# Kernel tuning notes

Hardware: AMD Instinct MI355X
Metric: run time of the kernel (lower is better)

## Reference

```python
import jax, jax.numpy as jnp
import numpy as np

B, N_GENES, N_SETS, G = 256, 10000, 1000, 128   # batch, input_dim, output_dim, geneset_size
H1, H2 = 64, 32                                  # hidden_dims
EPS = 1e-5                                       # BatchNorm1d eps


def _batchnorm(h, gamma, beta):
    # BatchNorm1d in training mode: biased batch stats over the batch axis
    mean = jnp.mean(h, axis=0, keepdims=True)
    var = jnp.mean(jnp.square(h - mean), axis=0, keepdims=True)
    return (h - mean) * jax.lax.rsqrt(var + EPS) * gamma + beta


def setup_inputs() -> dict:
    key = jax.random.key(0)
    ks = jax.random.split(key, 7)
    # Adjacency with exactly G distinct ones per column -> gather index list [N_SETS, G]
    rng = np.random.default_rng(0)
    gene_idx = np.argsort(rng.random((N_SETS, N_GENES)), axis=1)[:, :G]
    gene_idx = jnp.asarray(np.sort(gene_idx, axis=1), dtype=jnp.int32)

    x = jax.random.normal(ks[0], (B, N_GENES), jnp.float32)
    s1, s2, s3 = 1.0 / np.sqrt(G), 1.0 / np.sqrt(H1), 1.0 / np.sqrt(H2)
    W1 = jax.random.uniform(ks[1], (N_SETS, G, H1), jnp.float32, -s1, s1)
    b1 = jax.random.uniform(ks[2], (N_SETS, H1), jnp.float32, -s1, s1)
    W2 = jax.random.uniform(ks[3], (N_SETS, H1, H2), jnp.float32, -s2, s2)
    b2 = jax.random.uniform(ks[4], (N_SETS, H2), jnp.float32, -s2, s2)
    W3 = jax.random.uniform(ks[5], (N_SETS, H2), jnp.float32, -s3, s3)
    b3 = jax.random.uniform(ks[6], (N_SETS,), jnp.float32, -s3, s3)
    g1 = jnp.ones((N_SETS, H1), jnp.float32)
    be1 = jnp.zeros((N_SETS, H1), jnp.float32)
    g2 = jnp.ones((N_SETS, H2), jnp.float32)
    be2 = jnp.zeros((N_SETS, H2), jnp.float32)
    return {"x": x, "gene_idx": gene_idx, "W1": W1, "b1": b1, "g1": g1, "be1": be1,
            "W2": W2, "b2": b2, "g2": g2, "be2": be2, "W3": W3, "b3": b3}


def reference(x, gene_idx, W1, b1, g1, be1, W2, b2, g2, be2, W3, b3):
    # Per-geneset gather: x[:, adj[:,i]==1] for all i at once -> [B, S, G]
    xg = x[:, gene_idx]
    # Linear -> ReLU -> BatchNorm (per geneset, grouped GEMM)
    h = jax.nn.relu(jnp.einsum('bsg,sgh->bsh', xg, W1) + b1)
    h = _batchnorm(h, g1, be1)
    h = jax.nn.relu(jnp.einsum('bsh,shk->bsk', h, W2) + b2)
    h = _batchnorm(h, g2, be2)
    # Final Linear(H2 -> 1) -> ReLU, concatenated over genesets -> [B, S]
    out = jax.nn.relu(jnp.einsum('bsh,sh->bs', h, W3) + b3)
    return out
```

## Files before the change

### kernel.cpp

```cpp
#include <hip/hip_runtime.h>
#include <stdint.h>

#define BB 256
#define NG 10000
#define NS 1000
#define GG 128
#define H1 64
#define H2 32
#define EPSV 1e-5f


typedef unsigned short ushortT;
typedef __attribute__((ext_vector_type(4))) short short4v;
typedef __attribute__((ext_vector_type(8))) short short8v;
typedef __attribute__((ext_vector_type(4))) float float4v;

__device__ __forceinline__ float bf2f(ushortT u) {
    union { uint32_t i; float f; } v; v.i = ((uint32_t)u) << 16; return v.f;
}
__device__ __forceinline__ ushortT f2bf(float f) {
    union { float f; uint32_t i; } v; v.f = f;
    uint32_t x = v.i;
    return (ushortT)((x + 0x7fffu + ((x >> 16) & 1u)) >> 16);
}
__device__ __forceinline__ uint32_t pack2(ushortT lo, ushortT hi) {
    return (uint32_t)lo | ((uint32_t)hi << 16);
}
__device__ __forceinline__ bool probe_f32(const void* g1) {
    return ((*(const uint32_t*)g1) & 0xFFFFu) == 0u;
}
__device__ __forceinline__ float loadf(const void* p, int i, bool isf) {
    return isf ? ((const float*)p)[i] : bf2f(((const ushortT*)p)[i]);
}
__device__ __forceinline__ ushortT loadbf(const void* p, size_t i, bool isf) {
    return isf ? f2bf(((const float*)p)[i]) : ((const ushortT*)p)[i];
}

__global__ __launch_bounds__(256) void k_transpose(const void* __restrict__ x,
                                                   ushortT* __restrict__ xT,
                                                   const void* __restrict__ g1p) {
    __shared__ ushortT tile[64][66];
    const bool isf = probe_f32(g1p);
    const int tx = threadIdx.x & 63;
    const int tz = threadIdx.x >> 6;
    const int j0 = blockIdx.x * 64;
    const int b0 = blockIdx.y * 64;
    const int j = j0 + tx;
#pragma unroll
    for (int k = 0; k < 16; ++k) {
        int bl = tz * 16 + k;
        ushortT v = 0;
        if (j < NG) v = loadbf(x, (size_t)(b0 + bl) * NG + j, isf);
        tile[bl][tx] = v;
    }
    __syncthreads();
#pragma unroll
    for (int k = 0; k < 16; ++k) {
        int jl = tz * 16 + k;
        int jw = j0 + jl;
        if (jw < NG) xT[jw * BB + b0 + tx] = tile[tx][jl];
    }
}

__global__ __launch_bounds__(256, 3) void k_main(
    const ushortT* __restrict__ xT, const int* __restrict__ gidx,
    const void* __restrict__ W1, const void* __restrict__ W2,
    const void* __restrict__ b1, const void* __restrict__ g1, const void* __restrict__ be1,
    const void* __restrict__ b2, const void* __restrict__ g2, const void* __restrict__ be2,
    const void* __restrict__ W3, const void* __restrict__ b3,
    void* __restrict__ out) {
    __shared__ ushortT xg[BB * 72];
    __shared__ ushortT w1s[H1 * 132];

    char* xgc = (char*)xg;
    float* colA  = (float*)w1s;
    float* colB  = colA + 64;
    float* colA2 = colB + 64;
    float* colB2 = colA2 + 32;
    ushortT* w2s = w1s + 1408;

    const bool isf = probe_f32(g1);
    const int s = blockIdx.x;
    const int t = threadIdx.x;
    const int w = t >> 6;
    const int lane = t & 63;
    const int l16 = lane & 15;
    const int quad = lane >> 4;
    const size_t base1 = (size_t)s * (GG * H1);
    const size_t base2 = (size_t)s * (H1 * H2);

    float b1v[4], w3v[2], b2v[2];
#pragma unroll
    for (int nt = 0; nt < 4; ++nt) b1v[nt] = loadf(b1, s * H1 + nt * 16 + l16, isf);
#pragma unroll
    for (int nt = 0; nt < 2; ++nt) {
        b2v[nt] = loadf(b2, s * H2 + nt * 16 + l16, isf);
        w3v[nt] = loadf(W3, s * H2 + nt * 16 + l16, isf);
    }
    const float b3v = loadf(b3, s, isf);
    float g1v = 0.f, be1v = 0.f, g2v = 0.f, be2v = 0.f;
    if (t < 64) { g1v = loadf(g1, s * H1 + t, isf); be1v = loadf(be1, s * H1 + t, isf); }
    if (t < 32) { g2v = loadf(g2, s * H2 + t, isf); be2v = loadf(be2, s * H2 + t, isf); }

    ushortT w2r[8];
    {
        const int k2 = t & 31, h0 = (t >> 5) * 8;
#pragma unroll
        for (int j = 0; j < 8; ++j) w2r[j] = loadbf(W2, base2 + (size_t)(h0 + j) * H2 + k2, isf);
    }

    if (t < GG) *(int*)(xgc + (t >> 2) * 144 + 128 + (t & 3) * 4) = gidx[s * GG + t];

    if (isf) {
        const float4* src = (const float4*)((const float*)W1 + base1);
#pragma unroll
        for (int rep = 0; rep < 8; ++rep) {
            const int e4 = rep * 256 + t;
            const int g = e4 >> 4;
            const int h0 = (e4 & 15) * 4;
            float4 v = src[e4];
            w1s[(h0 + 0) * 132 + g] = f2bf(v.x);
            w1s[(h0 + 1) * 132 + g] = f2bf(v.y);
            w1s[(h0 + 2) * 132 + g] = f2bf(v.z);
            w1s[(h0 + 3) * 132 + g] = f2bf(v.w);
        }
    } else {
        const uint2* src = (const uint2*)((const ushortT*)W1 + base1);
#pragma unroll
        for (int rep = 0; rep < 8; ++rep) {
            const int e4 = rep * 256 + t;
            const int g = e4 >> 4;
            const int h0 = (e4 & 15) * 4;
            uint2 v = src[e4];
            w1s[(h0 + 0) * 132 + g] = (ushortT)v.x;
            w1s[(h0 + 1) * 132 + g] = (ushortT)(v.x >> 16);
            w1s[(h0 + 2) * 132 + g] = (ushortT)v.y;
            w1s[(h0 + 3) * 132 + g] = (ushortT)(v.y >> 16);
        }
    }
    __syncthreads();

    float4v acc1[4][4];
#pragma unroll
    for (int mt = 0; mt < 4; ++mt)
#pragma unroll
        for (int nt = 0; nt < 4; ++nt) acc1[mt][nt] = (float4v){0.f, 0.f, 0.f, 0.f};

#pragma unroll
    for (int c = 0; c < 2; ++c) {
#pragma unroll
        for (int gq = 0; gq < 8; ++gq) {
            const int r0 = c * 16 + gq * 2;
            int4 ia = *(const int4*)(xgc + r0 * 144 + 128);
            int4 ib = *(const int4*)(xgc + (r0 + 1) * 144 + 128);
            ushortT v0 = xT[ia.x * BB + t], v1 = xT[ia.y * BB + t];
            ushortT v2 = xT[ia.z * BB + t], v3 = xT[ia.w * BB + t];
            ushortT v4 = xT[ib.x * BB + t], v5 = xT[ib.y * BB + t];
            ushortT v6 = xT[ib.z * BB + t], v7 = xT[ib.w * BB + t];
            uint4 pk;
            pk.x = pack2(v0, v1);
            pk.y = pack2(v2, v3);
            pk.z = pack2(v4, v5);
            pk.w = pack2(v6, v7);
            *(uint4*)(&xg[t * 72 + gq * 8]) = pk;
        }
#pragma unroll
        for (int kt = 0; kt < 2; ++kt) {
            const int kl = kt * 32 + quad * 8;
            short8v bfrag[4];
#pragma unroll
            for (int nt = 0; nt < 4; ++nt) {
                const int h = nt * 16 + l16;
                const int woff = h * 132 + c * 64 + kl;
                short4v blo = *(const short4v*)(&w1s[woff]);
                short4v bhi = *(const short4v*)(&w1s[woff + 4]);
                bfrag[nt] = __builtin_shufflevector(blo, bhi, 0, 1, 2, 3, 4, 5, 6, 7);
            }
#pragma unroll
            for (int mt = 0; mt < 4; ++mt) {
                const int b = w * 64 + mt * 16 + l16;
                short8v af = *(const short8v*)(&xg[b * 72 + kl]);
#pragma unroll
                for (int nt = 0; nt < 4; ++nt)
                    acc1[mt][nt] = __builtin_amdgcn_mfma_f32_16x16x32_bf16(af, bfrag[nt], acc1[mt][nt], 0, 0, 0);
            }
        }
    }

#pragma unroll
    for (int nt = 0; nt < 4; ++nt) {
        float s1 = 0.f, s2 = 0.f;
        const float bb = b1v[nt];
#pragma unroll
        for (int mt = 0; mt < 4; ++mt)
#pragma unroll
            for (int r = 0; r < 4; ++r) {
                float v = acc1[mt][nt][r] + bb;
                v = v > 0.f ? v : 0.f;
                s1 += v;
                s2 += v * v;
            }
        s1 += __shfl_xor(s1, 16); s1 += __shfl_xor(s1, 32);
        s2 += __shfl_xor(s2, 16); s2 += __shfl_xor(s2, 32);
        if (lane < 16) {
            const int k = w * 64 + nt * 16 + lane;
            *(float*)(xgc + (32 + (k >> 2)) * 144 + 128 + (k & 3) * 4) = s1;
            *(float*)(xgc + (96 + (k >> 2)) * 144 + 128 + (k & 3) * 4) = s2;
        }
    }
    __syncthreads();

    if (t < 64) {
        float ts = 0.f, tq = 0.f;
#pragma unroll
        for (int ww = 0; ww < 4; ++ww) {
            const int k = ww * 64 + t;
            ts += *(const float*)(xgc + (32 + (k >> 2)) * 144 + 128 + (k & 3) * 4);
            tq += *(const float*)(xgc + (96 + (k >> 2)) * 144 + 128 + (k & 3) * 4);
        }
        float mean = ts * (1.0f / 256.0f);
        float var = tq * (1.0f / 256.0f) - mean * mean;
        var = var > 0.f ? var : 0.f;
        float rs = rsqrtf(var + EPSV);
        float a = g1v * rs;
        colA[t] = a;
        colB[t] = be1v - mean * a;
    }
    {
        const int k2 = t & 31, h0 = (t >> 5) * 8;
        uint4 pk;
        pk.x = pack2(w2r[0], w2r[1]);
        pk.y = pack2(w2r[2], w2r[3]);
        pk.z = pack2(w2r[4], w2r[5]);
        pk.w = pack2(w2r[6], w2r[7]);
        *(uint4*)(&w2s[k2 * 72 + h0]) = pk;
    }
    __syncthreads();

#pragma unroll
    for (int nt = 0; nt < 4; ++nt) {
        const int h = nt * 16 + l16;
        const float bb = b1v[nt], a = colA[h], cc = colB[h];
#pragma unroll
        for (int mt = 0; mt < 4; ++mt)
#pragma unroll
            for (int r = 0; r < 4; ++r) {
                const int b = w * 64 + mt * 16 + quad * 4 + r;
                float v = acc1[mt][nt][r] + bb;
                v = v > 0.f ? v : 0.f;
                xg[b * 72 + h] = f2bf(v * a + cc);
            }
    }

    float4v acc2[4][2];
#pragma unroll
    for (int mt = 0; mt < 4; ++mt)
#pragma unroll
        for (int nt = 0; nt < 2; ++nt) acc2[mt][nt] = (float4v){0.f, 0.f, 0.f, 0.f};

#pragma unroll
    for (int kt = 0; kt < 2; ++kt) {
        const int kl = kt * 32 + quad * 8;
        short8v bfrag2[2];
#pragma unroll
        for (int nt = 0; nt < 2; ++nt) {
            const int k2 = nt * 16 + l16;
            bfrag2[nt] = *(const short8v*)(&w2s[k2 * 72 + kl]);
        }
#pragma unroll
        for (int mt = 0; mt < 4; ++mt) {
            const int b = w * 64 + mt * 16 + l16;
            short8v af = *(const short8v*)(&xg[b * 72 + kl]);
#pragma unroll
            for (int nt = 0; nt < 2; ++nt)
                acc2[mt][nt] = __builtin_amdgcn_mfma_f32_16x16x32_bf16(af, bfrag2[nt], acc2[mt][nt], 0, 0, 0);
        }
    }

#pragma unroll
    for (int nt = 0; nt < 2; ++nt) {
        float s1 = 0.f, s2 = 0.f;
        const float bb = b2v[nt];
#pragma unroll
        for (int mt = 0; mt < 4; ++mt)
#pragma unroll
            for (int r = 0; r < 4; ++r) {
                float v = acc2[mt][nt][r] + bb;
                v = v > 0.f ? v : 0.f;
                s1 += v;
                s2 += v * v;
            }
        s1 += __shfl_xor(s1, 16); s1 += __shfl_xor(s1, 32);
        s2 += __shfl_xor(s2, 16); s2 += __shfl_xor(s2, 32);
        if (lane < 16) {
            const int k = w * 64 + nt * 16 + lane;
            *(float*)(xgc + (32 + (k >> 2)) * 144 + 128 + (k & 3) * 4) = s1;
            *(float*)(xgc + (96 + (k >> 2)) * 144 + 128 + (k & 3) * 4) = s2;
        }
    }
    __syncthreads();

    if (t < 32) {
        float ts = 0.f, tq = 0.f;
#pragma unroll
        for (int ww = 0; ww < 4; ++ww) {
            const int k = ww * 64 + t;
            ts += *(const float*)(xgc + (32 + (k >> 2)) * 144 + 128 + (k & 3) * 4);
            tq += *(const float*)(xgc + (96 + (k >> 2)) * 144 + 128 + (k & 3) * 4);
        }
        float mean = ts * (1.0f / 256.0f);
        float var = tq * (1.0f / 256.0f) - mean * mean;
        var = var > 0.f ? var : 0.f;
        float rs = rsqrtf(var + EPSV);
        float a = g2v * rs;
        colA2[t] = a;
        colB2[t] = be2v - mean * a;
    }
    __syncthreads();

    float a2[2], c2[2];
#pragma unroll
    for (int nt = 0; nt < 2; ++nt) {
        const int k2 = nt * 16 + l16;
        a2[nt] = colA2[k2];
        c2[nt] = colB2[k2];
    }
#pragma unroll
    for (int mt = 0; mt < 4; ++mt)
#pragma unroll
        for (int r = 0; r < 4; ++r) {
            float tot = 0.f;
#pragma unroll
            for (int nt = 0; nt < 2; ++nt) {
                float v = acc2[mt][nt][r] + b2v[nt];
                v = v > 0.f ? v : 0.f;
                tot += (v * a2[nt] + c2[nt]) * w3v[nt];
            }
            tot += __shfl_xor(tot, 1);
            tot += __shfl_xor(tot, 2);
            tot += __shfl_xor(tot, 4);
            tot += __shfl_xor(tot, 8);
            if (l16 == 0) {
                const int b = w * 64 + mt * 16 + quad * 4 + r;
                float o = tot + b3v;
                o = o > 0.f ? o : 0.f;
                if (isf) ((float*)out)[b * NS + s] = o;
                else     ((ushortT*)out)[b * NS + s] = f2bf(o);
            }
        }
}

extern "C" void kernel_launch(void* const* d_in, const int* in_sizes, int n_in,
                              void* d_out, int out_size, void* d_ws, size_t ws_size,
                              hipStream_t stream) {
    const int* gi = (const int*)d_in[1];
    ushortT* xT = (ushortT*)d_ws;

    dim3 gT((NG + 63) / 64, BB / 64);
    k_transpose<<<gT, 256, 0, stream>>>(d_in[0], xT, d_in[4]);
    k_main<<<NS, 256, 0, stream>>>(xT, gi, d_in[2], d_in[6],
                                   d_in[3], d_in[4], d_in[5],
                                   d_in[7], d_in[8], d_in[9], d_in[10], d_in[11],
                                   d_out);
}
```

Baseline: 147.7 us.

## Shrink LDS footprint by staging W1 in K-quarters to raise occupancy

Reduces shared memory per block by staging W1 into LDS one 32-wide K slice at a time instead of all 128, and narrowing the xg row pitch from 72 to 68. Reduction scratch moves into the padding holes of the xg rows and into the reused W1 buffer. Launch bounds go from 3 to 4 blocks per CU to exploit the smaller footprint. In exchange there are extra __syncthreads and global W1 reloads inside the K loop, plus split 8-byte LDS reads where 16-byte reads were used before.

Result: faster. 141.9 us (-3.9%).

```diff
diff --git a/kernel.cpp b/kernel.cpp
--- a/kernel.cpp
+++ b/kernel.cpp
@@ -62,22 +62,19 @@
     }
 }
 
-__global__ __launch_bounds__(256, 3) void k_main(
+__global__ __launch_bounds__(256, 4) void k_main(
     const ushortT* __restrict__ xT, const int* __restrict__ gidx,
     const void* __restrict__ W1, const void* __restrict__ W2,
     const void* __restrict__ b1, const void* __restrict__ g1, const void* __restrict__ be1,
     const void* __restrict__ b2, const void* __restrict__ g2, const void* __restrict__ be2,
     const void* __restrict__ W3, const void* __restrict__ b3,
     void* __restrict__ out) {
-    __shared__ ushortT xg[BB * 72];
-    __shared__ ushortT w1s[H1 * 132];
+    __shared__ ushortT xg[BB * 68];
+    __shared__ ushortT w1s[64 * 36];
 
     char* xgc = (char*)xg;
-    float* colA  = (float*)w1s;
-    float* colB  = colA + 64;
-    float* colA2 = colB + 64;
-    float* colB2 = colA2 + 32;
-    ushortT* w2s = w1s + 1408;
+    float* redf = (float*)w1s;
+    ushortT* w2s = w1s;
 
     const bool isf = probe_f32(g1);
     const int s = blockIdx.x;
@@ -89,6 +86,9 @@
     const size_t base1 = (size_t)s * (GG * H1);
     const size_t base2 = (size_t)s * (H1 * H2);
 
+#define HOLEI(i)   (*(int*)(xgc + ((i) >> 1) * 136 + 128 + ((i) & 1) * 4))
+#define HOLEF(r0, k) (*(float*)(xgc + ((r0) + ((k) >> 1)) * 136 + 128 + ((k) & 1) * 4))
+
     float b1v[4], w3v[2], b2v[2];
 #pragma unroll
     for (int nt = 0; nt < 4; ++nt) b1v[nt] = loadf(b1, s * H1 + nt * 16 + l16, isf);
@@ -109,35 +109,31 @@
         for (int j = 0; j < 8; ++j) w2r[j] = loadbf(W2, base2 + (size_t)(h0 + j) * H2 + k2, isf);
     }
 
-    if (t < GG) *(int*)(xgc + (t >> 2) * 144 + 128 + (t & 3) * 4) = gidx[s * GG + t];
-
-    if (isf) {
-        const float4* src = (const float4*)((const float*)W1 + base1);
-#pragma unroll
-        for (int rep = 0; rep < 8; ++rep) {
-            const int e4 = rep * 256 + t;
-            const int g = e4 >> 4;
-            const int h0 = (e4 & 15) * 4;
-            float4 v = src[e4];
-            w1s[(h0 + 0) * 132 + g] = f2bf(v.x);
-            w1s[(h0 + 1) * 132 + g] = f2bf(v.y);
-            w1s[(h0 + 2) * 132 + g] = f2bf(v.z);
-            w1s[(h0 + 3) * 132 + g] = f2bf(v.w);
-        }
-    } else {
-        const uint2* src = (const uint2*)((const ushortT*)W1 + base1);
-#pragma unroll
-        for (int rep = 0; rep < 8; ++rep) {
-            const int e4 = rep * 256 + t;
-            const int g = e4 >> 4;
-            const int h0 = (e4 & 15) * 4;
-            uint2 v = src[e4];
-            w1s[(h0 + 0) * 132 + g] = (ushortT)v.x;
-            w1s[(h0 + 1) * 132 + g] = (ushortT)(v.x >> 16);
-            w1s[(h0 + 2) * 132 + g] = (ushortT)v.y;
-            w1s[(h0 + 3) * 132 + g] = (ushortT)(v.y >> 16);
-        }
-    }
+    if (t < GG) HOLEI(t) = gidx[s * GG + t];
+
+    auto stageW1 = [&](int q) {
+#pragma unroll
+        for (int rep = 0; rep < 2; ++rep) {
+            const int el = rep * 256 + t;
+            const int e4 = q * 512 + el;
+            const int g = el >> 4;
+            const int h0 = (el & 15) * 4;
+            ushortT u0, u1, u2, u3;
+            if (isf) {
+                float4 v = *(const float4*)((const float*)W1 + base1 + (size_t)e4 * 4);
+                u0 = f2bf(v.x); u1 = f2bf(v.y); u2 = f2bf(v.z); u3 = f2bf(v.w);
+            } else {
+                uint2 v = *(const uint2*)((const ushortT*)W1 + base1 + (size_t)e4 * 4);
+                u0 = (ushortT)v.x; u1 = (ushortT)(v.x >> 16);
+                u2 = (ushortT)v.y; u3 = (ushortT)(v.y >> 16);
+            }
+            w1s[(h0 + 0) * 36 + g] = u0;
+            w1s[(h0 + 1) * 36 + g] = u1;
+            w1s[(h0 + 2) * 36 + g] = u2;
+            w1s[(h0 + 3) * 36 + g] = u3;
+        }
+    };
+    stageW1(0);
     __syncthreads();
 
     float4v acc1[4][4];
@@ -150,28 +146,33 @@
     for (int c = 0; c < 2; ++c) {
 #pragma unroll
         for (int gq = 0; gq < 8; ++gq) {
-            const int r0 = c * 16 + gq * 2;
-            int4 ia = *(const int4*)(xgc + r0 * 144 + 128);
-            int4 ib = *(const int4*)(xgc + (r0 + 1) * 144 + 128);
-            ushortT v0 = xT[ia.x * BB + t], v1 = xT[ia.y * BB + t];
-            ushortT v2 = xT[ia.z * BB + t], v3 = xT[ia.w * BB + t];
-            ushortT v4 = xT[ib.x * BB + t], v5 = xT[ib.y * BB + t];
-            ushortT v6 = xT[ib.z * BB + t], v7 = xT[ib.w * BB + t];
-            uint4 pk;
-            pk.x = pack2(v0, v1);
-            pk.y = pack2(v2, v3);
-            pk.z = pack2(v4, v5);
-            pk.w = pack2(v6, v7);
-            *(uint4*)(&xg[t * 72 + gq * 8]) = pk;
+            const int i0 = c * 64 + gq * 8;
+            int2 p0 = *(const int2*)(xgc + (i0 >> 1) * 136 + 128);
+            int2 p1 = *(const int2*)(xgc + ((i0 >> 1) + 1) * 136 + 128);
+            int2 p2 = *(const int2*)(xgc + ((i0 >> 1) + 2) * 136 + 128);
+            int2 p3 = *(const int2*)(xgc + ((i0 >> 1) + 3) * 136 + 128);
+            ushortT v0 = xT[p0.x * BB + t], v1 = xT[p0.y * BB + t];
+            ushortT v2 = xT[p1.x * BB + t], v3 = xT[p1.y * BB + t];
+            ushortT v4 = xT[p2.x * BB + t], v5 = xT[p2.y * BB + t];
+            ushortT v6 = xT[p3.x * BB + t], v7 = xT[p3.y * BB + t];
+            uint2 pa = {pack2(v0, v1), pack2(v2, v3)};
+            uint2 pb = {pack2(v4, v5), pack2(v6, v7)};
+            *(uint2*)(&xg[t * 68 + gq * 8]) = pa;
+            *(uint2*)(&xg[t * 68 + gq * 8 + 4]) = pb;
         }
 #pragma unroll
         for (int kt = 0; kt < 2; ++kt) {
-            const int kl = kt * 32 + quad * 8;
+            const int q = 2 * c + kt;
+            if (q > 0) {
+                __syncthreads();
+                stageW1(q);
+                __syncthreads();
+            }
             short8v bfrag[4];
 #pragma unroll
             for (int nt = 0; nt < 4; ++nt) {
                 const int h = nt * 16 + l16;
-                const int woff = h * 132 + c * 64 + kl;
+                const int woff = h * 36 + quad * 8;
                 short4v blo = *(const short4v*)(&w1s[woff]);
                 short4v bhi = *(const short4v*)(&w1s[woff + 4]);
                 bfrag[nt] = __builtin_shufflevector(blo, bhi, 0, 1, 2, 3, 4, 5, 6, 7);
@@ -179,7 +180,10 @@
 #pragma unroll
             for (int mt = 0; mt < 4; ++mt) {
                 const int b = w * 64 + mt * 16 + l16;
-                short8v af = *(const short8v*)(&xg[b * 72 + kl]);
+                const ushortT* p = &xg[b * 68 + kt * 32 + quad * 8];
+                short4v alo = *(const short4v*)(p);
+                short4v ahi = *(const short4v*)(p + 4);
+                short8v af = __builtin_shufflevector(alo, ahi, 0, 1, 2, 3, 4, 5, 6, 7);
 #pragma unroll
                 for (int nt = 0; nt < 4; ++nt)
                     acc1[mt][nt] = __builtin_amdgcn_mfma_f32_16x16x32_bf16(af, bfrag[nt], acc1[mt][nt], 0, 0, 0);
@@ -187,6 +191,7 @@
         }
     }
 
+    float s1v[4], s2v[4];
 #pragma unroll
     for (int nt = 0; nt < 4; ++nt) {
         float s1 = 0.f, s2 = 0.f;
@@ -202,30 +207,32 @@
             }
         s1 += __shfl_xor(s1, 16); s1 += __shfl_xor(s1, 32);
         s2 += __shfl_xor(s2, 16); s2 += __shfl_xor(s2, 32);
-        if (lane < 16) {
+        s1v[nt] = s1; s2v[nt] = s2;
+    }
+    __syncthreads();
+    if (lane < 16) {
+#pragma unroll
+        for (int nt = 0; nt < 4; ++nt) {
             const int k = w * 64 + nt * 16 + lane;
-            *(float*)(xgc + (32 + (k >> 2)) * 144 + 128 + (k & 3) * 4) = s1;
-            *(float*)(xgc + (96 + (k >> 2)) * 144 + 128 + (k & 3) * 4) = s2;
+            redf[k] = s1v[nt];
+            redf[256 + k] = s2v[nt];
         }
     }
     __syncthreads();
 
     if (t < 64) {
-        float ts = 0.f, tq = 0.f;
-#pragma unroll
-        for (int ww = 0; ww < 4; ++ww) {
-            const int k = ww * 64 + t;
-            ts += *(const float*)(xgc + (32 + (k >> 2)) * 144 + 128 + (k & 3) * 4);
-            tq += *(const float*)(xgc + (96 + (k >> 2)) * 144 + 128 + (k & 3) * 4);
-        }
+        float ts = redf[t] + redf[64 + t] + redf[128 + t] + redf[192 + t];
+        float tq = redf[256 + t] + redf[320 + t] + redf[384 + t] + redf[448 + t];
         float mean = ts * (1.0f / 256.0f);
         float var = tq * (1.0f / 256.0f) - mean * mean;
         var = var > 0.f ? var : 0.f;
         float rs = rsqrtf(var + EPSV);
         float a = g1v * rs;
-        colA[t] = a;
-        colB[t] = be1v - mean * a;
-    }
+        HOLEF(64, t) = a;
+        HOLEF(96, t) = be1v - mean * a;
+    }
+    __syncthreads();
+
     {
         const int k2 = t & 31, h0 = (t >> 5) * 8;
         uint4 pk;
@@ -235,12 +242,11 @@
         pk.w = pack2(w2r[6], w2r[7]);
         *(uint4*)(&w2s[k2 * 72 + h0]) = pk;
     }
-    __syncthreads();
-
 #pragma unroll
     for (int nt = 0; nt < 4; ++nt) {
         const int h = nt * 16 + l16;
-        const float bb = b1v[nt], a = colA[h], cc = colB[h];
+        const float bb = b1v[nt];
+        const float a = HOLEF(64, h), cc = HOLEF(96, h);
 #pragma unroll
         for (int mt = 0; mt < 4; ++mt)
 #pragma unroll
@@ -248,9 +254,10 @@
                 const int b = w * 64 + mt * 16 + quad * 4 + r;
                 float v = acc1[mt][nt][r] + bb;
                 v = v > 0.f ? v : 0.f;
-                xg[b * 72 + h] = f2bf(v * a + cc);
-            }
-    }
+                xg[b * 68 + h] = f2bf(v * a + cc);
+            }
+    }
+    __syncthreads();
 
     float4v acc2[4][2];
 #pragma unroll
@@ -265,12 +272,18 @@
 #pragma unroll
         for (int nt = 0; nt < 2; ++nt) {
             const int k2 = nt * 16 + l16;
-            bfrag2[nt] = *(const short8v*)(&w2s[k2 * 72 + kl]);
+            const int woff = k2 * 72 + kl;
+            short4v blo = *(const short4v*)(&w2s[woff]);
+            short4v bhi = *(const short4v*)(&w2s[woff + 4]);
+            bfrag2[nt] = __builtin_shufflevector(blo, bhi, 0, 1, 2, 3, 4, 5, 6, 7);
         }
 #pragma unroll
         for (int mt = 0; mt < 4; ++mt) {
             const int b = w * 64 + mt * 16 + l16;
-            short8v af = *(const short8v*)(&xg[b * 72 + kl]);
+            const ushortT* p = &xg[b * 68 + kl];
+            short4v alo = *(const short4v*)(p);
+            short4v ahi = *(const short4v*)(p + 4);
+            short8v af = __builtin_shufflevector(alo, ahi, 0, 1, 2, 3, 4, 5, 6, 7);
 #pragma unroll
             for (int nt = 0; nt < 2; ++nt)
                 acc2[mt][nt] = __builtin_amdgcn_mfma_f32_16x16x32_bf16(af, bfrag2[nt], acc2[mt][nt], 0, 0, 0);
@@ -293,28 +306,23 @@
         s1 += __shfl_xor(s1, 16); s1 += __shfl_xor(s1, 32);
         s2 += __shfl_xor(s2, 16); s2 += __shfl_xor(s2, 32);
         if (lane < 16) {
-            const int k = w * 64 + nt * 16 + lane;
-            *(float*)(xgc + (32 + (k >> 2)) * 144 + 128 + (k & 3) * 4) = s1;
-            *(float*)(xgc + (96 + (k >> 2)) * 144 + 128 + (k & 3) * 4) = s2;
+            const int k = w * 32 + nt * 16 + lane;
+            HOLEF(0, k) = s1;
+            HOLEF(64, k) = s2;
         }
     }
     __syncthreads();
 
     if (t < 32) {
-        float ts = 0.f, tq = 0.f;
-#pragma unroll
-        for (int ww = 0; ww < 4; ++ww) {
-            const int k = ww * 64 + t;
-            ts += *(const float*)(xgc + (32 + (k >> 2)) * 144 + 128 + (k & 3) * 4);
-            tq += *(const float*)(xgc + (96 + (k >> 2)) * 144 + 128 + (k & 3) * 4);
-        }
+        float ts = HOLEF(0, t) + HOLEF(0, 32 + t) + HOLEF(0, 64 + t) + HOLEF(0, 96 + t);
+        float tq = HOLEF(64, t) + HOLEF(64, 32 + t) + HOLEF(64, 64 + t) + HOLEF(64, 96 + t);
         float mean = ts * (1.0f / 256.0f);
         float var = tq * (1.0f / 256.0f) - mean * mean;
         var = var > 0.f ? var : 0.f;
         float rs = rsqrtf(var + EPSV);
         float a = g2v * rs;
-        colA2[t] = a;
-        colB2[t] = be2v - mean * a;
+        HOLEF(128, t) = a;
+        HOLEF(144, t) = be2v - mean * a;
     }
     __syncthreads();
 
@@ -322,8 +330,8 @@
 #pragma unroll
     for (int nt = 0; nt < 2; ++nt) {
         const int k2 = nt * 16 + l16;
-        a2[nt] = colA2[k2];
-        c2[nt] = colB2[k2];
+        a2[nt] = HOLEF(128, k2);
+        c2[nt] = HOLEF(144, k2);
     }
 #pragma unroll
     for (int mt = 0; mt < 4; ++mt)
@@ -348,6 +356,8 @@
                 else     ((ushortT*)out)[b * NS + s] = f2bf(o);
             }
         }
+#undef HOLEI
+#undef HOLEF
 }
 
 extern "C" void kernel_launch(void* const* d_in, const int* in_sizes, int n_in,
```
